# Optimization experiments

Hardware: AMD Instinct MI355X
Metric: run time of the kernel (lower is better)

Reference implementation:

```python
import jax, jax.numpy as jnp
import numpy as np
import math

DIM = 1024
N_HEADS = 16
HEAD_DIM = DIM // N_HEADS  # 64
GROUP = 128
B, T = 2, 2048
ROPE_THETA = 10000.0


def bitlinear(x, w, group_size=GROUP):
    """BitLinear (BitNet b1.58 style) forward: per-group ternary weight quant +
    per-token int8 absmax activation quant. STE is irrelevant in fwd-only."""
    O, I = w.shape
    wg = w.reshape(O, I // group_size, group_size)
    ws = jnp.mean(jnp.abs(wg), axis=-1, keepdims=True) + 1e-5
    wq = (jnp.clip(jnp.round(wg / ws), -1.0, 1.0) * ws).reshape(O, I)
    s = 127.0 / (jnp.max(jnp.abs(x), axis=-1, keepdims=True) + 1e-5)
    xq = jnp.clip(jnp.round(x * s), -128.0, 127.0) / s
    return jnp.einsum('bti,oi->bto', xq, wq)


def rope(x, cos, sin):
    # x: [B,T,H,D]; cos/sin: [T,D/2]; complex mult on interleaved pairs
    xs = x.reshape(*x.shape[:-1], -1, 2)
    xe, xo = xs[..., 0], xs[..., 1]
    c = cos[None, :, None, :]
    s = sin[None, :, None, :]
    oe = xe * c - xo * s
    oo = xe * s + xo * c
    return jnp.stack([oe, oo], axis=-1).reshape(x.shape)


def setup_inputs() -> dict:
    key = jax.random.key(0)
    ks = jax.random.split(key, 5)
    x = jax.random.normal(ks[0], (B, T, DIM), dtype=jnp.float32)
    wq_w = jax.random.normal(ks[1], (DIM, DIM), dtype=jnp.float32) * 0.02
    wk_w = jax.random.normal(ks[2], (DIM, DIM), dtype=jnp.float32) * 0.02
    wv_w = jax.random.normal(ks[3], (DIM, DIM), dtype=jnp.float32) * 0.02
    wo_w = jax.random.normal(ks[4], (DIM, DIM), dtype=jnp.float32) * 0.02
    # precompute freqs_cis (as cos/sin) like standard RoPE
    inv = 1.0 / (ROPE_THETA ** (np.arange(0, HEAD_DIM, 2, dtype=np.float32) / HEAD_DIM))
    ang = np.arange(T, dtype=np.float32)[:, None] * inv[None, :]  # [T, D/2]
    return {
        'x': x,
        'cos': jnp.asarray(np.cos(ang)),
        'sin': jnp.asarray(np.sin(ang)),
        'wq_w': wq_w, 'wk_w': wk_w, 'wv_w': wv_w, 'wo_w': wo_w,
    }


def reference(x, cos, sin, wq_w, wk_w, wv_w, wo_w):
    Bb, Tt, _ = x.shape
    q = bitlinear(x, wq_w).reshape(Bb, Tt, N_HEADS, HEAD_DIM)
    k = bitlinear(x, wk_w).reshape(Bb, Tt, N_HEADS, HEAD_DIM)
    v = bitlinear(x, wv_w).reshape(Bb, Tt, N_HEADS, HEAD_DIM)
    q = rope(q, cos, sin)
    k = rope(k, cos, sin)
    # [B,H,T,D]
    q = q.transpose(0, 2, 1, 3)
    k = k.transpose(0, 2, 1, 3)
    v = v.transpose(0, 2, 1, 3)
    attn = jnp.einsum('bhqd,bhkd->bhqk', q, k) / math.sqrt(HEAD_DIM)
    causal = jnp.tril(jnp.ones((Tt, Tt), dtype=bool))
    attn = jnp.where(causal[None, None], attn, -jnp.inf)
    attn = jax.nn.softmax(attn, axis=-1)
    out = jnp.einsum('bhqk,bhkd->bhqd', attn, v)
    out = out.transpose(0, 2, 1, 3).reshape(Bb, Tt, -1)
    return bitlinear(out, wo_w)
```

## Files before the change

kernel.cpp:

```cpp
#include <hip/hip_runtime.h>
#include <math.h>

#define DIM   1024
#define NH    16
#define HD    64
#define GRP   128
#define BB    2
#define TT    2048
#define MROWS (BB*TT)

typedef __attribute__((ext_vector_type(8))) short s16x8;
typedef __attribute__((ext_vector_type(4))) float f32x4;
typedef __attribute__((ext_vector_type(4))) int   i32x4;
typedef __attribute__((ext_vector_type(16))) int  i32x16;

__device__ inline float wave_max(float v){
    for(int off=32; off; off>>=1) v = fmaxf(v, __shfl_xor(v, off));
    return v;
}

__device__ inline unsigned short f2bf(float x){
    union { float f; unsigned u; } v; v.f = x;
    unsigned r = v.u + 0x7fffu + ((v.u >> 16) & 1u);
    return (unsigned short)(r >> 16);
}

#if __has_builtin(__builtin_amdgcn_cvt_pk_bf16_f32)
typedef __bf16 bf16x2 __attribute__((ext_vector_type(2)));
__device__ inline unsigned pk2(float a, float b){
    union { bf16x2 v; unsigned u; } c;
    c.v = __builtin_amdgcn_cvt_pk_bf16_f32(a, b);
    return c.u;
}
#else
__device__ inline unsigned pk2(float a, float b){
    return (unsigned)f2bf(a) | ((unsigned)f2bf(b) << 16);
}
#endif

#if __has_builtin(__builtin_amdgcn_exp2f)
__device__ inline float fexp2(float x){ return __builtin_amdgcn_exp2f(x); }
#else
__device__ inline float fexp2(float x){ return exp2f(x); }
#endif

__device__ inline i32x16 zero16(){
    i32x16 z;
    #pragma unroll
    for(int i=0;i<16;i++) z[i]=0;
    return z;
}

__device__ inline void gload16(const void* g, void* l){
    __builtin_amdgcn_global_load_lds((const __attribute__((address_space(1))) unsigned int*)g,
                                     (__attribute__((address_space(3))) unsigned int*)l, 16, 0, 0);
}

#define QSC 0.18033688011112042f

__global__ __launch_bounds__(256) void quant_all(const float* __restrict__ x,
                                                 const float* __restrict__ w0,
                                                 const float* __restrict__ w1,
                                                 const float* __restrict__ w2,
                                                 const float* __restrict__ w3,
                                                 char* __restrict__ w8,
                                                 float* __restrict__ wsall,
                                                 char* __restrict__ xq8,
                                                 float* __restrict__ srow){
    int blk = blockIdx.x;
    int tid = threadIdx.x;
    if (blk < 1024){
        int widx = blk >> 8;
        const float* w = (widx==0)?w0 : (widx==1)?w1 : (widx==2)?w2 : w3;
        int gloc = (blk & 255)*32 + (tid >> 3);
        int j = tid & 7;
        const float* p = w + (size_t)gloc*GRP;
        float r = 0.f;
        #pragma unroll
        for(int i=0;i<16;i++) r += fabsf(p[8*i + j]);
        r += __shfl_xor(r, 1);
        r += __shfl_xor(r, 2);
        r += __shfl_xor(r, 4);
        float ws = r/(float)GRP + 1e-5f;
        if (j == 0) wsall[widx*8192 + gloc] = ws;
        int* q = (int*)(w8 + (size_t)widx*1048576 + (size_t)gloc*GRP);
        int i0 = j*16;
        #pragma unroll
        for(int c4=0;c4<4;c4++){
            float4 v = *(const float4*)(p + i0 + c4*4);
            int b0 = (int)fminf(fmaxf(rintf(v.x/ws),-1.f),1.f);
            int b1 = (int)fminf(fmaxf(rintf(v.y/ws),-1.f),1.f);
            int b2 = (int)fminf(fmaxf(rintf(v.z/ws),-1.f),1.f);
            int b3 = (int)fminf(fmaxf(rintf(v.w/ws),-1.f),1.f);
            q[j*4 + c4] = (b0&0xff) | ((b1&0xff)<<8) | ((b2&0xff)<<16) | ((b3&0xff)<<24);
        }
    } else {
        int row = blk - 1024;
        const float* p = x + (size_t)row*DIM;
        float4 v = *(const float4*)(p + tid*4);
        float m = fmaxf(fmaxf(fabsf(v.x),fabsf(v.y)), fmaxf(fabsf(v.z),fabsf(v.w)));
        m = wave_max(m);
        __shared__ float red[4];
        if ((tid&63)==0) red[tid>>6] = m;
        __syncthreads();
        m = fmaxf(fmaxf(red[0],red[1]), fmaxf(red[2],red[3]));
        float s = 127.f/(m+1e-5f);
        int a0 = (int)fminf(fmaxf(rintf(v.x*s),-128.f),127.f);
        int a1 = (int)fminf(fmaxf(rintf(v.y*s),-128.f),127.f);
        int a2 = (int)fminf(fmaxf(rintf(v.z*s),-128.f),127.f);
        int a3 = (int)fminf(fmaxf(rintf(v.w*s),-128.f),127.f);
        int pk = (a0&0xff) | ((a1&0xff)<<8) | ((a2&0xff)<<16) | ((a3&0xff)<<24);
        ((int*)xq8)[(size_t)row*256 + tid] = pk;
        if (tid==0) srow[row] = s;
    }
}

__global__ __launch_bounds__(256) void quant_x_i8(const float* __restrict__ x,
                                                  char* __restrict__ xq8,
                                                  float* __restrict__ srow){
    int row = blockIdx.x;
    int tid = threadIdx.x;
    const float* p = x + (size_t)row*DIM;
    float4 v = *(const float4*)(p + tid*4);
    float m = fmaxf(fmaxf(fabsf(v.x),fabsf(v.y)), fmaxf(fabsf(v.z),fabsf(v.w)));
    m = wave_max(m);
    __shared__ float red[4];
    if ((tid&63)==0) red[tid>>6] = m;
    __syncthreads();
    m = fmaxf(fmaxf(red[0],red[1]), fmaxf(red[2],red[3]));
    float s = 127.f/(m+1e-5f);
    int a0 = (int)fminf(fmaxf(rintf(v.x*s),-128.f),127.f);
    int a1 = (int)fminf(fmaxf(rintf(v.y*s),-128.f),127.f);
    int a2 = (int)fminf(fmaxf(rintf(v.z*s),-128.f),127.f);
    int a3 = (int)fminf(fmaxf(rintf(v.w*s),-128.f),127.f);
    int pk = (a0&0xff) | ((a1&0xff)<<8) | ((a2&0xff)<<16) | ((a3&0xff)<<24);
    ((int*)xq8)[(size_t)row*256 + tid] = pk;
    if (tid==0) srow[row] = s;
}

__device__ inline void kloop_i8(const char* __restrict__ Arow,
                                const char* __restrict__ Brow0,
                                const char* __restrict__ Brow1,
                                const float wsr[2][8],
                                float facc[2][16]){
    int lh = (threadIdx.x & 63) >> 5;
    #pragma unroll
    for(int g=0; g<8; g++){
        i32x16 iacc[2];
        iacc[0]=zero16(); iacc[1]=zero16();
        #pragma unroll
        for(int s=0; s<4; s++){
            int off = g*128 + (s*2 + lh)*16;
            i32x4 afr = *(const i32x4*)(Arow  + off);
            i32x4 b0  = *(const i32x4*)(Brow0 + off);
            i32x4 b1  = *(const i32x4*)(Brow1 + off);
            iacc[0] = __builtin_amdgcn_mfma_i32_32x32x32_i8(afr, b0, iacc[0], 0, 0, 0);
            iacc[1] = __builtin_amdgcn_mfma_i32_32x32x32_i8(afr, b1, iacc[1], 0, 0, 0);
        }
        #pragma unroll
        for(int jt=0; jt<2; jt++)
            #pragma unroll
            for(int r=0;r<16;r++)
                facc[jt][r] += (float)iacc[jt][r] * wsr[jt][g];
    }
}

__global__ __launch_bounds__(256) void gemm_qkv(const char* __restrict__ A8,
                                                const char* __restrict__ w8all,
                                                const float* __restrict__ wsall,
                                                const float* __restrict__ srow,
                                                const float* __restrict__ cosb,
                                                const float* __restrict__ sinb,
                                                unsigned short* __restrict__ Qh,
                                                unsigned short* __restrict__ Kf,
                                                unsigned short* __restrict__ Vf){
    __shared__ float T[64*132];

    int nt = blockIdx.x;
    int widx = nt >> 3;
    int n0 = (nt & 7)*128;
    int m0 = blockIdx.y*64;
    const char* W8 = w8all + (size_t)widx*1048576;
    const float* wsb = wsall + widx*8192;

    int tid = threadIdx.x;
    int w = tid >> 6, lane = tid & 63;
    int wm = w & 1, wn = w >> 1;
    int l31 = lane & 31, lh = lane >> 5;

    float wsr[2][8];
    #pragma unroll
    for(int jt=0; jt<2; jt++){
        int col = n0 + (wn*2+jt)*32 + l31;
        float4 q0 = *(const float4*)(wsb + (size_t)col*8);
        float4 q1 = *(const float4*)(wsb + (size_t)col*8 + 4);
        wsr[jt][0]=q0.x; wsr[jt][1]=q0.y; wsr[jt][2]=q0.z; wsr[jt][3]=q0.w;
        wsr[jt][4]=q1.x; wsr[jt][5]=q1.y; wsr[jt][6]=q1.z; wsr[jt][7]=q1.w;
    }

    float facc[2][16];
    #pragma unroll
    for(int b=0;b<2;b++)
        #pragma unroll
        for(int r=0;r<16;r++) facc[b][r]=0.f;

    const char* Arow  = A8 + (size_t)(m0 + wm*32 + l31)*1024;
    const char* Brow0 = W8 + (size_t)(n0 + wn*64 + l31)*1024;
    const char* Brow1 = Brow0 + 32*1024;
    kloop_i8(Arow, Brow0, Brow1, wsr, facc);

    #pragma unroll
    for(int r=0; r<16; r++){
        int rowl = wm*32 + (r&3) + 8*(r>>2) + 4*lh;
        float sv = srow[m0 + rowl];
        #pragma unroll
        for(int jt=0; jt<2; jt++){
            int col = (wn*2+jt)*32 + l31;
            T[rowl*132 + col] = facc[jt][r] / sv;
        }
    }
    __syncthreads();

    int kt = (m0 & (TT-1)) >> 6;
    int bglob = m0 >> 11;
    int h0 = n0 >> 6;

    if (widx == 0){
        int row = tid & 63, chunk = tid >> 6;
        int t = (m0 + row) & (TT-1);
        const float* Tr = T + row*132 + chunk*32;
        int colbase = n0 + chunk*32;
        int h = colbase >> 6;
        int d0 = colbase & 63;
        int bh = bglob*NH + h;
        unsigned short* dst = Qh + ((size_t)bh*TT + t)*HD + d0;
        int p0 = d0 >> 1;
        __align__(16) unsigned short ob[32];
        #pragma unroll
        for(int pp=0; pp<16; pp++){
            float c = cosb[t*32 + p0 + pp], s = sinb[t*32 + p0 + pp];
            float e = Tr[2*pp], o = Tr[2*pp+1];
            ob[2*pp]   = f2bf((e*c - o*s)*QSC);
            ob[2*pp+1] = f2bf((e*s + o*c)*QSC);
        }
        #pragma unroll
        for(int c4=0;c4<4;c4++)
            *(s16x8*)(dst + c4*8) = *(s16x8*)(ob + c4*8);
    } else if (widx == 1){
        #pragma unroll
        for(int i=0;i<4;i++){
            int e = tid + 256*i;
            int h = e >> 9, e2 = e & 511;
            int f = e2 >> 7, cc = (e2 >> 6)&1, gg = (e2 >> 4)&3, mm = e2 & 15;
            int row = 16*f + mm;
            int t = (m0 + row) & (TT-1);
            int d0 = 8*gg + 32*cc;
            const float* Tr = T + row*132 + h*64 + d0;
            int p0 = d0 >> 1;
            __align__(16) unsigned short ob[8];
            #pragma unroll
            for(int pp=0;pp<4;pp++){
                float c = cosb[t*32 + p0 + pp], s = sinb[t*32 + p0 + pp];
                float ev = Tr[2*pp], ov = Tr[2*pp+1];
                ob[2*pp]   = f2bf(ev*c - ov*s);
                ob[2*pp+1] = f2bf(ev*s + ov*c);
            }
            int bh = bglob*NH + h0 + h;
            size_t entry = ((size_t)(bh*32 + kt))*512 + e2;
            *(s16x8*)(Kf + entry*8) = *(s16x8*)ob;
        }
    } else {
        #pragma unroll
        for(int i=0;i<4;i++){
            int e = tid + 256*i;
            int h = e >> 9, e2 = e & 511;
            int f = e2 >> 7, cc = (e2 >> 6)&1, gg = (e2 >> 4)&3, mm = e2 & 15;
            int dv = 16*f + mm;
            int tl0 = 8*gg + 32*cc;
            __align__(16) unsigned short ob[8];
            #pragma unroll
            for(int j=0;j<8;j++)
                ob[j] = f2bf(T[(tl0+j)*132 + h*64 + dv]);
            int bh = bglob*NH + h0 + h;
            size_t entry = ((size_t)(bh*32 + kt))*512 + e2;
            *(s16x8*)(Vf + entry*8) = *(s16x8*)ob;
        }
    }
}

__global__ __launch_bounds__(256) void gemm_i8(const char* __restrict__ A8,
                                               const char* __restrict__ W8,
                                               const float* __restrict__ wsb,
                                               const float* __restrict__ srow,
                                               float* __restrict__ C){
    int tid = threadIdx.x;
    int w = tid >> 6, lane = tid & 63;
    int wm = w & 1, wn = w >> 1;
    int m0 = blockIdx.y*64, n0 = blockIdx.x*128;
    int l31 = lane & 31, lh = lane >> 5;

    float wsr[2][8];
    #pragma unroll
    for(int jt=0; jt<2; jt++){
        int col = n0 + (wn*2+jt)*32 + l31;
        float4 q0 = *(const float4*)(wsb + (size_t)col*8);
        float4 q1 = *(const float4*)(wsb + (size_t)col*8 + 4);
        wsr[jt][0]=q0.x; wsr[jt][1]=q0.y; wsr[jt][2]=q0.z; wsr[jt][3]=q0.w;
        wsr[jt][4]=q1.x; wsr[jt][5]=q1.y; wsr[jt][6]=q1.z; wsr[jt][7]=q1.w;
    }

    float facc[2][16];
    #pragma unroll
    for(int b=0;b<2;b++)
        #pragma unroll
        for(int r=0;r<16;r++) facc[b][r]=0.f;

    const char* Arow  = A8 + (size_t)(m0 + wm*32 + l31)*1024;
    const char* Brow0 = W8 + (size_t)(n0 + wn*64 + l31)*1024;
    const char* Brow1 = Brow0 + 32*1024;
    kloop_i8(Arow, Brow0, Brow1, wsr, facc);

    #pragma unroll
    for(int r=0; r<16; r++){
        int rowl = wm*32 + (r&3) + 8*(r>>2) + 4*lh;
        float sv = srow[m0 + rowl];
        #pragma unroll
        for(int jt=0; jt<2; jt++){
            int col = n0 + (wn*2+jt)*32 + l31;
            C[(size_t)(m0+rowl)*DIM + col] = facc[jt][r] / sv;
        }
    }
}

__global__ __launch_bounds__(256) void attn_mfma3(const unsigned short* __restrict__ Qh,
                                                  const unsigned short* __restrict__ Kf,
                                                  const unsigned short* __restrict__ Vf,
                                                  float* __restrict__ ao){
    __shared__ s16x8 Kbuf[2][512];
    __shared__ s16x8 Vbuf[2][512];
    int blk = blockIdx.x;
    int qt = 31 - (blk >> 5);
    int bh = blk & 31;
    int b  = bh >> 4;
    int tid = threadIdx.x;
    int w = tid >> 6, lane = tid & 63;
    int m = lane & 15, g = lane >> 4;
    int q = qt*64 + w*16 + m;

    const unsigned short* Qhead = Qh + (size_t)bh*TT*HD;
    const char* Kbase = (const char*)(Kf + (size_t)bh*32*4096);
    const char* Vbase = (const char*)(Vf + (size_t)bh*32*4096);

    s16x8 Qf0 = *(const s16x8*)(Qhead + (size_t)q*HD + g*8);
    s16x8 Qf1 = *(const s16x8*)(Qhead + (size_t)q*HD + g*8 + 32);

    f32x4 Of[4] = {f32x4{0,0,0,0}, f32x4{0,0,0,0}, f32x4{0,0,0,0}, f32x4{0,0,0,0}};
    float mrow = -1e30f, lrow = 0.f;

    #pragma unroll
    for(int r=0;r<2;r++){
        gload16(Kbase + ((r*4 + w)*64 + lane)*16, (char*)Kbuf[0] + (r*4 + w)*1024);
        gload16(Vbase + ((r*4 + w)*64 + lane)*16, (char*)Vbuf[0] + (r*4 + w)*1024);
    }

    for(int kt=0; kt<=qt; kt++){
        __syncthreads();
        if (kt < qt){
            int nb = (kt+1)&1;
            size_t goff = (size_t)(kt+1)*8192;
            #pragma unroll
            for(int r=0;r<2;r++){
                gload16(Kbase + goff + ((r*4 + w)*64 + lane)*16, (char*)Kbuf[nb] + (r*4 + w)*1024);
                gload16(Vbase + goff + ((r*4 + w)*64 + lane)*16, (char*)Vbuf[nb] + (r*4 + w)*1024);
            }
        }
        const s16x8* Kc = Kbuf[kt&1];
        const s16x8* Vc = Vbuf[kt&1];

        f32x4 S[4];
        #pragma unroll
        for(int f=0; f<4; f++){
            s16x8 k0 = Kc[(f*2+0)*64 + lane];
            s16x8 k1 = Kc[(f*2+1)*64 + lane];
            f32x4 acc = {0,0,0,0};
            acc = __builtin_amdgcn_mfma_f32_16x16x32_bf16(k0, Qf0, acc, 0, 0, 0);
            acc = __builtin_amdgcn_mfma_f32_16x16x32_bf16(k1, Qf1, acc, 0, 0, 0);
            S[f] = acc;
        }

        float p[4][4];
        float mloc = -1e30f;
        if (kt == qt){
            #pragma unroll
            for(int f=0; f<4; f++)
                #pragma unroll
                for(int r=0; r<4; r++){
                    int key = 16*f + 4*g + r;
                    float s = (qt*64 + key > q) ? -1e30f : S[f][r];
                    p[f][r] = s;
                    mloc = fmaxf(mloc, s);
                }
        } else {
            #pragma unroll
            for(int f=0; f<4; f++)
                #pragma unroll
                for(int r=0; r<4; r++){
                    p[f][r] = S[f][r];
                    mloc = fmaxf(mloc, S[f][r]);
                }
        }
        mloc = fmaxf(mloc, __shfl_xor(mloc, 16));
        mloc = fmaxf(mloc, __shfl_xor(mloc, 32));
        float mn = fmaxf(mrow, mloc);
        float alpha = fexp2(mrow - mn);
        float ps = 0.f;
        #pragma unroll
        for(int f=0; f<4; f++)
            #pragma unroll
            for(int r=0; r<4; r++){
                float e = fexp2(p[f][r] - mn);
                p[f][r] = e;
                ps += e;
            }
        ps += __shfl_xor(ps, 16);
        ps += __shfl_xor(ps, 32);
        lrow = lrow*alpha + ps;
        mrow = mn;

        #pragma unroll
        for(int f2=0; f2<4; f2++)
            #pragma unroll
            for(int r=0; r<4; r++) Of[f2][r] *= alpha;

        unsigned pp0[4], pp1[4];
        #pragma unroll
        for(int f=0; f<4; f++){
            pp0[f] = pk2(p[f][0], p[f][1]);
            pp1[f] = pk2(p[f][2], p[f][3]);
        }

        int src0 = m + 16*(2*(g&1));
        int src1 = src0 + 16;
        bool hi = (g >= 2);
        #pragma unroll
        for(int c=0; c<2; c++){
            unsigned a0 = (unsigned)__shfl((int)pp0[2*c],   src0);
            unsigned a1 = (unsigned)__shfl((int)pp0[2*c+1], src0);
            unsigned b0 = hi ? a1 : a0;
            unsigned a2 = (unsigned)__shfl((int)pp1[2*c],   src0);
            unsigned a3 = (unsigned)__shfl((int)pp1[2*c+1], src0);
            unsigned b1 = hi ? a3 : a2;
            unsigned a4 = (unsigned)__shfl((int)pp0[2*c],   src1);
            unsigned a5 = (unsigned)__shfl((int)pp0[2*c+1], src1);
            unsigned b2 = hi ? a5 : a4;
            unsigned a6 = (unsigned)__shfl((int)pp1[2*c],   src1);
            unsigned a7 = (unsigned)__shfl((int)pp1[2*c+1], src1);
            unsigned b3 = hi ? a7 : a6;
            union { unsigned u[4]; s16x8 v; } Bf;
            Bf.u[0]=b0; Bf.u[1]=b1; Bf.u[2]=b2; Bf.u[3]=b3;
            #pragma unroll
            for(int f2=0; f2<4; f2++){
                s16x8 vf = Vc[(f2*2+c)*64 + lane];
                Of[f2] = __builtin_amdgcn_mfma_f32_16x16x32_bf16(vf, Bf.v, Of[f2], 0, 0, 0);
            }
        }
    }

    float invl = 1.0f / lrow;
    size_t obase = (size_t)(b*TT + q)*DIM + (bh & 15)*HD;
    #pragma unroll
    for(int f2=0; f2<4; f2++)
        #pragma unroll
        for(int r=0; r<4; r++)
            ao[obase + 16*f2 + 4*g + r] = Of[f2][r]*invl;
}

extern "C" void kernel_launch(void* const* d_in, const int* in_sizes, int n_in,
                              void* d_out, int out_size, void* d_ws, size_t ws_size,
                              hipStream_t stream){
    const float* x    = (const float*)d_in[0];
    const float* cosb = (const float*)d_in[1];
    const float* sinb = (const float*)d_in[2];
    const float* wq_w = (const float*)d_in[3];
    const float* wk_w = (const float*)d_in[4];
    const float* wv_w = (const float*)d_in[5];
    const float* wo_w = (const float*)d_in[6];
    float* out = (float*)d_out;

    char* cw = (char*)d_ws;
    const size_t MB = 1048576;
    char*  w8all = cw;
    float* wsall = (float*)(cw + 4*MB);
    float* srow1 = (float*)(cw + 4*MB + 131072);
    float* srow2 = (float*)(cw + 4*MB + 147456);
    char*  xq8   = cw + 5*MB;
    char*  xq8_2 = cw + 9*MB;
    unsigned short* Qh = (unsigned short*)(cw + 13*MB);
    unsigned short* Kf = (unsigned short*)(cw + 21*MB);
    unsigned short* Vf = (unsigned short*)(cw + 29*MB);
    float* ao    = (float*)(cw + 37*MB);

    quant_all<<<1024 + MROWS, 256, 0, stream>>>(x, wq_w, wk_w, wv_w, wo_w,
                                                w8all, wsall, xq8, srow1);

    gemm_qkv<<<dim3(24, MROWS/64), 256, 0, stream>>>(xq8, w8all, wsall, srow1,
                                                     cosb, sinb, Qh, Kf, Vf);

    attn_mfma3<<<1024, 256, 0, stream>>>(Qh, Kf, Vf, ao);

    quant_x_i8<<<MROWS, 256, 0, stream>>>(ao, xq8_2, srow2);
    gemm_i8<<<dim3(DIM/128, MROWS/64), 256, 0, stream>>>(xq8_2, w8all + 3*MB,
                                                         wsall + 3*8192, srow2, out);
}
```

Baseline: 246.7 us.

## Pack int8 activations and weights in MFMA fragment order for coalesced loads

The quantization kernels now write int8 activations and ternary weights in a tiled layout where each 32-row block stores MFMA fragments contiguously, indexed by group, k-step and lane. The GEMM inner loop then reads each fragment as one contiguous 1 KB chunk per wave instead of 16-byte pieces strided by 1 KB across rows. This targets poorly coalesced global loads in the QKV and output GEMMs. In exchange, the quant kernels do scattered 4-byte stores, and the packed format is tied to the 32x32x32 MFMA operand layout.

```diff
diff --git a/kernel.cpp b/kernel.cpp
--- a/kernel.cpp
+++ b/kernel.cpp
@@ -58,14 +58,15 @@
 
 #define QSC 0.18033688011112042f
 
+
 __global__ __launch_bounds__(256) void quant_all(const float* __restrict__ x,
                                                  const float* __restrict__ w0,
                                                  const float* __restrict__ w1,
                                                  const float* __restrict__ w2,
                                                  const float* __restrict__ w3,
-                                                 char* __restrict__ w8,
+                                                 char* __restrict__ wpk,
                                                  float* __restrict__ wsall,
-                                                 char* __restrict__ xq8,
+                                                 char* __restrict__ xpk,
                                                  float* __restrict__ srow){
     int blk = blockIdx.x;
     int tid = threadIdx.x;
@@ -83,7 +84,9 @@
         r += __shfl_xor(r, 4);
         float ws = r/(float)GRP + 1e-5f;
         if (j == 0) wsall[widx*8192 + gloc] = ws;
-        int* q = (int*)(w8 + (size_t)widx*1048576 + (size_t)gloc*GRP);
+        int n = gloc >> 3, g = gloc & 7;
+        char* base = wpk + (size_t)widx*1048576 + (size_t)(n>>5)*32768
+                   + (size_t)(((g*4 + (j>>1))*64 + ((j&1)*32 + (n&31)))*16);
         int i0 = j*16;
         #pragma unroll
         for(int c4=0;c4<4;c4++){
@@ -92,7 +95,7 @@
             int b1 = (int)fminf(fmaxf(rintf(v.y/ws),-1.f),1.f);
             int b2 = (int)fminf(fmaxf(rintf(v.z/ws),-1.f),1.f);
             int b3 = (int)fminf(fmaxf(rintf(v.w/ws),-1.f),1.f);
-            q[j*4 + c4] = (b0&0xff) | ((b1&0xff)<<8) | ((b2&0xff)<<16) | ((b3&0xff)<<24);
+            *(int*)(base + c4*4) = (b0&0xff) | ((b1&0xff)<<8) | ((b2&0xff)<<16) | ((b3&0xff)<<24);
         }
     } else {
         int row = blk - 1024;
@@ -110,13 +113,16 @@
         int a2 = (int)fminf(fmaxf(rintf(v.z*s),-128.f),127.f);
         int a3 = (int)fminf(fmaxf(rintf(v.w*s),-128.f),127.f);
         int pk = (a0&0xff) | ((a1&0xff)<<8) | ((a2&0xff)<<16) | ((a3&0xff)<<24);
-        ((int*)xq8)[(size_t)row*256 + tid] = pk;
+        int g = tid >> 5, chunk = (tid&31) >> 2;
+        *(int*)(xpk + (size_t)(row>>5)*32768
+               + (size_t)(((g*4 + (chunk>>1))*64 + ((chunk&1)*32 + (row&31)))*16)
+               + (tid&3)*4) = pk;
         if (tid==0) srow[row] = s;
     }
 }
 
 __global__ __launch_bounds__(256) void quant_x_i8(const float* __restrict__ x,
-                                                  char* __restrict__ xq8,
+                                                  char* __restrict__ xpk,
                                                   float* __restrict__ srow){
     int row = blockIdx.x;
     int tid = threadIdx.x;
@@ -134,26 +140,29 @@
     int a2 = (int)fminf(fmaxf(rintf(v.z*s),-128.f),127.f);
     int a3 = (int)fminf(fmaxf(rintf(v.w*s),-128.f),127.f);
     int pk = (a0&0xff) | ((a1&0xff)<<8) | ((a2&0xff)<<16) | ((a3&0xff)<<24);
-    ((int*)xq8)[(size_t)row*256 + tid] = pk;
+    int g = tid >> 5, chunk = (tid&31) >> 2;
+    *(int*)(xpk + (size_t)(row>>5)*32768
+           + (size_t)(((g*4 + (chunk>>1))*64 + ((chunk&1)*32 + (row&31)))*16)
+           + (tid&3)*4) = pk;
     if (tid==0) srow[row] = s;
 }
 
-__device__ inline void kloop_i8(const char* __restrict__ Arow,
-                                const char* __restrict__ Brow0,
-                                const char* __restrict__ Brow1,
+__device__ inline void kloop_pk(const char* __restrict__ A,
+                                const char* __restrict__ B0,
+                                const char* __restrict__ B1,
                                 const float wsr[2][8],
                                 float facc[2][16]){
-    int lh = (threadIdx.x & 63) >> 5;
+    int lane = threadIdx.x & 63;
     #pragma unroll
     for(int g=0; g<8; g++){
         i32x16 iacc[2];
         iacc[0]=zero16(); iacc[1]=zero16();
         #pragma unroll
         for(int s=0; s<4; s++){
-            int off = g*128 + (s*2 + lh)*16;
-            i32x4 afr = *(const i32x4*)(Arow  + off);
-            i32x4 b0  = *(const i32x4*)(Brow0 + off);
-            i32x4 b1  = *(const i32x4*)(Brow1 + off);
+            size_t off = (size_t)(((g*4+s)*64 + lane)*16);
+            i32x4 afr = *(const i32x4*)(A  + off);
+            i32x4 b0  = *(const i32x4*)(B0 + off);
+            i32x4 b1  = *(const i32x4*)(B1 + off);
             iacc[0] = __builtin_amdgcn_mfma_i32_32x32x32_i8(afr, b0, iacc[0], 0, 0, 0);
             iacc[1] = __builtin_amdgcn_mfma_i32_32x32x32_i8(afr, b1, iacc[1], 0, 0, 0);
         }
@@ -165,8 +174,8 @@
     }
 }
 
-__global__ __launch_bounds__(256) void gemm_qkv(const char* __restrict__ A8,
-                                                const char* __restrict__ w8all,
+__global__ __launch_bounds__(256) void gemm_qkv(const char* __restrict__ Apk,
+                                                const char* __restrict__ wpk,
                                                 const float* __restrict__ wsall,
                                                 const float* __restrict__ srow,
                                                 const float* __restrict__ cosb,
@@ -180,7 +189,7 @@
     int widx = nt >> 3;
     int n0 = (nt & 7)*128;
     int m0 = blockIdx.y*64;
-    const char* W8 = w8all + (size_t)widx*1048576;
+    const char* W = wpk + (size_t)widx*1048576;
     const float* wsb = wsall + widx*8192;
 
     int tid = threadIdx.x;
@@ -204,10 +213,10 @@
         #pragma unroll
         for(int r=0;r<16;r++) facc[b][r]=0.f;
 
-    const char* Arow  = A8 + (size_t)(m0 + wm*32 + l31)*1024;
-    const char* Brow0 = W8 + (size_t)(n0 + wn*64 + l31)*1024;
-    const char* Brow1 = Brow0 + 32*1024;
-    kloop_i8(Arow, Brow0, Brow1, wsr, facc);
+    const char* A  = Apk + (size_t)((m0>>5) + wm)*32768;
+    const char* B0 = W   + (size_t)((n0>>5) + wn*2)*32768;
+    const char* B1 = B0 + 32768;
+    kloop_pk(A, B0, B1, wsr, facc);
 
     #pragma unroll
     for(int r=0; r<16; r++){
@@ -288,8 +297,8 @@
     }
 }
 
-__global__ __launch_bounds__(256) void gemm_i8(const char* __restrict__ A8,
-                                               const char* __restrict__ W8,
+__global__ __launch_bounds__(256) void gemm_i8(const char* __restrict__ Apk,
+                                               const char* __restrict__ Wp,
                                                const float* __restrict__ wsb,
                                                const float* __restrict__ srow,
                                                float* __restrict__ C){
@@ -315,10 +324,10 @@
         #pragma unroll
         for(int r=0;r<16;r++) facc[b][r]=0.f;
 
-    const char* Arow  = A8 + (size_t)(m0 + wm*32 + l31)*1024;
-    const char* Brow0 = W8 + (size_t)(n0 + wn*64 + l31)*1024;
-    const char* Brow1 = Brow0 + 32*1024;
-    kloop_i8(Arow, Brow0, Brow1, wsr, facc);
+    const char* A  = Apk + (size_t)((m0>>5) + wm)*32768;
+    const char* B0 = Wp  + (size_t)((n0>>5) + wn*2)*32768;
+    const char* B1 = B0 + 32768;
+    kloop_pk(A, B0, B1, wsr, facc);
 
     #pragma unroll
     for(int r=0; r<16; r++){
@@ -489,26 +498,26 @@
 
     char* cw = (char*)d_ws;
     const size_t MB = 1048576;
-    char*  w8all = cw;
+    char*  wpk   = cw;
     float* wsall = (float*)(cw + 4*MB);
     float* srow1 = (float*)(cw + 4*MB + 131072);
     float* srow2 = (float*)(cw + 4*MB + 147456);
-    char*  xq8   = cw + 5*MB;
-    char*  xq8_2 = cw + 9*MB;
+    char*  xpk   = cw + 5*MB;
+    char*  xpk2  = cw + 9*MB;
     unsigned short* Qh = (unsigned short*)(cw + 13*MB);
     unsigned short* Kf = (unsigned short*)(cw + 21*MB);
     unsigned short* Vf = (unsigned short*)(cw + 29*MB);
     float* ao    = (float*)(cw + 37*MB);
 
     quant_all<<<1024 + MROWS, 256, 0, stream>>>(x, wq_w, wk_w, wv_w, wo_w,
-                                                w8all, wsall, xq8, srow1);
-
-    gemm_qkv<<<dim3(24, MROWS/64), 256, 0, stream>>>(xq8, w8all, wsall, srow1,
+                                                wpk, wsall, xpk, srow1);
+
+    gemm_qkv<<<dim3(24, MROWS/64), 256, 0, stream>>>(xpk, wpk, wsall, srow1,
                                                      cosb, sinb, Qh, Kf, Vf);
 
     attn_mfma3<<<1024, 256, 0, stream>>>(Qh, Kf, Vf, ao);
 
-    quant_x_i8<<<MROWS, 256, 0, stream>>>(ao, xq8_2, srow2);
-    gemm_i8<<<dim3(DIM/128, MROWS/64), 256, 0, stream>>>(xq8_2, w8all + 3*MB,
+    quant_x_i8<<<MROWS, 256, 0, stream>>>(ao, xpk2, srow2);
+    gemm_i8<<<dim3(DIM/128, MROWS/64), 256, 0, stream>>>(xpk2, wpk + 3*MB,
                                                          wsall + 3*8192, srow2, out);
 }
```

New measurement: 201.3 us. 18.4% less time.
